# Kernel optimization log

Measured on AMD Instinct MI355X. Metric: run time of the kernel, lower is better.

The kernel has to match this reference:

```python
import jax, jax.numpy as jnp
import numpy as np

TEMPERATURE = 0.5  # set externally on the torch module; fixed here
EPS = 1e-10

B, NPTS, NDIM = 8, 1024, 64
K, S = 16, 512  # n_clusters, book_size


def setup_inputs() -> dict:
    key = jax.random.key(0)
    k1, k2, k3, k4 = jax.random.split(key, 4)
    ze = jax.random.normal(k1, (B, NPTS, NDIM), dtype=jnp.float32)
    # per-sample cluster probabilities (rows sum to 1)
    c_probs = jax.nn.softmax(jax.random.normal(k2, (B, K), dtype=jnp.float32), axis=-1)
    books = jax.random.normal(k3, (K, S, NDIM), dtype=jnp.float32)
    log_param_q = jnp.asarray(np.log(1.0), dtype=jnp.float32)  # param_q_init = 1.0
    gumbel_u = jax.random.uniform(k4, (B, K, NPTS, S), dtype=jnp.float32)
    return {"ze": ze, "c_probs": c_probs, "books": books,
            "log_param_q": log_param_q, "gumbel_u": gumbel_u}


def reference(ze, c_probs, books, log_param_q, gumbel_u):
    # precision of the Gaussian quantizer
    precision_q = 0.5 / jnp.clip(jnp.exp(log_param_q), 1e-10)
    # squared euclidean distances: [b, k, n, s]
    d = (jnp.sum(ze * ze, axis=-1)[:, None, :, None]
         + jnp.sum(books * books, axis=-1)[None, :, None, :]
         - 2.0 * jnp.einsum('bnd,ksd->bkns', ze, books))
    logits = -d * precision_q                                   # [b,k,n,s]
    # gumbel-softmax sample (training branch)
    g = -jnp.log(-jnp.log(gumbel_u + EPS) + EPS)
    encodings = jax.nn.softmax((logits + g) / TEMPERATURE, axis=-1)
    # soft codebook lookup, mixed over clusters by per-sample c_probs
    zq = jnp.einsum('bkns,ksd,bk->bnd', encodings, books, c_probs)
    prob = jax.nn.softmax(logits, axis=-1)
    log_prob = jax.nn.log_softmax(logits, axis=-1)
    return (zq, precision_q, prob, log_prob)
```

## Files before the change

### kernel.cpp

```cpp
#include <hip/hip_runtime.h>
#include <hip/hip_bf16.h>

typedef __attribute__((ext_vector_type(8))) short short8;
typedef __attribute__((ext_vector_type(4))) float f32x4;
typedef __attribute__((ext_vector_type(2))) float f32x2;

#define WS_ZE     0u
#define WS_B1H    (1u<<20)
#define WS_B2     (2u<<20)
#define WS_ZN2    (3u<<20)
#define WS_BS2    ((3u<<20)+32768u)
#define WS_ZQP    (4u<<20)

__device__ __forceinline__ unsigned short f2bf(float x) {
  __hip_bfloat16 h = __float2bfloat16(x);
  return __builtin_bit_cast(unsigned short, h);
}
__device__ __forceinline__ void lds_barrier() {
  asm volatile("s_waitcnt lgkmcnt(0)" ::: "memory");
  __builtin_amdgcn_s_barrier();
}

__global__ __launch_bounds__(256) void prep_all_k(const float* __restrict__ ze,
                                                  const float* __restrict__ books,
                                                  const float* __restrict__ lpq,
                                                  char* __restrict__ ws,
                                                  float* __restrict__ d_out) {
  const int bb = blockIdx.x;
  if (bb < 32) {
    int t = bb * 256 + threadIdx.x;
    const f32x4* row = (const f32x4*)(ze + t * 64);
    unsigned short* dh = (unsigned short*)(ws + WS_ZE) + t * 64;
    float s = 0.f;
#pragma unroll
    for (int c = 0; c < 8; ++c) {
      const f32x4 v0 = row[2 * c], v1 = row[2 * c + 1];
      union { unsigned short u[8]; short8 v; } H;
#pragma unroll
      for (int r = 0; r < 4; ++r) {
        float a = v0[r]; s += a * a; H.u[r] = f2bf(a);
        float b = v1[r]; s += b * b; H.u[4 + r] = f2bf(b);
      }
      *(short8*)(dh + c * 8) = H.v;
    }
    ((float*)(ws + WS_ZN2))[t] = s;
  } else if (bb < 64) {
    int t = (bb - 32) * 256 + threadIdx.x;
    if (t == 0) d_out[524288] = 0.5f / fmaxf(expf(lpq[0]), 1e-10f);
    const f32x4* row = (const f32x4*)(books + t * 64);
    float s = 0.f;
#pragma unroll
    for (int c = 0; c < 16; ++c) {
      const f32x4 v = row[c];
#pragma unroll
      for (int r = 0; r < 4; ++r) s += v[r] * v[r];
    }
    ((float*)(ws + WS_BS2))[t] = s;
  } else if (bb < 320) {
    int t = (bb - 64) * 256 + threadIdx.x;
    const int sl = t & 15, g = (t >> 4) & 3, f = (t >> 6) & 1, tt = (t >> 7) & 31, k = t >> 12;
    const float* src = books + ((k * 512 + tt * 16 + sl) * 64 + f * 32 + g * 8);
    const f32x4 v0 = *(const f32x4*)(src);
    const f32x4 v1 = *(const f32x4*)(src + 4);
    union { unsigned short u[8]; short8 v; } H;
#pragma unroll
    for (int r = 0; r < 4; ++r) { H.u[r] = f2bf(v0[r]); H.u[4 + r] = f2bf(v1[r]); }
    *(short8*)(ws + WS_B1H + (k * 32 + tt) * 2048 + f * 1024 + (sl + g * 16) * 16) = H.v;
  } else {
    int t = (bb - 320) * 256 + threadIdx.x;
    const int l15 = t & 15, sub = (t >> 4) & 3, m = (t >> 6) & 3, w = (t >> 8) & 7,
              hh = (t >> 11) & 1, k = t >> 12;
    const float* src = books + ((k * 512 + hh * 256 + w * 32 + sub * 8) * 64 + m * 16 + l15);
    union { unsigned short u[8]; short8 v; } H;
#pragma unroll
    for (int j = 0; j < 8; ++j) H.u[j] = f2bf(src[j * 64]);
    *(short8*)(ws + WS_B2 + k * 65536 + ((hh * 8 + w) * 4 + m) * 1024 + (l15 + sub * 16) * 16) = H.v;
  }
}

__global__ __launch_bounds__(256) void zq_red_k(const char* __restrict__ ws,
                                                float* __restrict__ d_out) {
  int t = blockIdx.x * 256 + threadIdx.x;
  const f32x4 a = *(const f32x4*)(ws + WS_ZQP + t * 16);
  const f32x4 b = *(const f32x4*)(ws + WS_ZQP + (2u << 20) + t * 16);
  const f32x4 c = *(const f32x4*)(ws + WS_ZQP + (4u << 20) + t * 16);
  const f32x4 d = *(const f32x4*)(ws + WS_ZQP + (6u << 20) + t * 16);
  *(f32x4*)(d_out + t * 4) = (a + b) + (c + d);
}

__global__ __launch_bounds__(512, 4)
void gvq_main(const float* __restrict__ gum, const float* __restrict__ cprobs,
              const float* __restrict__ lpq, char* __restrict__ ws,
              float* __restrict__ d_out) {
  __shared__ char lds[33088];
  char* lgb = lds;
  float* scr_esc = (float*)(lds + 33024);

  const int tid  = threadIdx.x;
  const int lane = tid & 63;
  const int wave = tid >> 6;
  const int l15  = lane & 15;
  const int g4   = lane >> 4;

  const int bid = blockIdx.x;
  const unsigned kg = ((unsigned)bid & 7u) >> 1;
  const int bt  = ((bid >> 3) << 1) | (bid & 1);
  const int b   = bt >> 6;
  const int n0  = (bt & 63) * 16;
  const int kbeg = (int)kg * 4;

  const float prec  = 0.5f / fmaxf(expf(lpq[0]), 1e-10f);
  const float prec2 = 2.0f * prec;
  const float C24   = 3.7751345442790977e-11f;

  const unsigned short* zh = (const unsigned short*)(ws + WS_ZE) + (b * 1024 + n0 + l15) * 64;
  const short8 zf0h = *(const short8*)(zh + g4 * 8);
  const short8 zf1h = *(const short8*)(zh + 32 + g4 * 8);
  const float zn2p = ((const float*)(ws + WS_ZN2))[b * 1024 + n0 + l15] * prec;

  f32x4 zacc[4] = {{0,0,0,0},{0,0,0,0},{0,0,0,0},{0,0,0,0}};

  const int nr0 = wave * 2, nr1 = wave * 2 + 1;

#pragma unroll 1
  for (int kk = 0; kk < 4; ++kk) {
    const int k = kbeg + kk;
    const float cp = cprobs[b * 16 + k];
    const char* b1h = ws + WS_B1H + k * 65536;
    const char* b2  = ws + WS_B2  + k * 65536;
    const float* bs2k = (const float*)(ws + WS_BS2) + k * 512;
    const long row0 = ((long)((b * 16 + k) * 1024) + n0 + nr0) * 512;
    const long row1 = ((long)((b * 16 + k) * 1024) + n0 + nr1) * 512;

#pragma unroll
    for (int i = 0; i < 4; ++i) {
      const int t = wave * 4 + i;
      const char* bh = b1h + t * 2048 + lane * 16;
      const short8 a0h = *(const short8*)(bh);
      const short8 a1h = *(const short8*)(bh + 1024);
      f32x4 c = {0.f, 0.f, 0.f, 0.f};
      c = __builtin_amdgcn_mfma_f32_16x16x32_bf16(a0h, zf0h, c, 0, 0, 0);
      c = __builtin_amdgcn_mfma_f32_16x16x32_bf16(a1h, zf1h, c, 0, 0, 0);
      const f32x4 bs2v = *(const f32x4*)(bs2k + t * 16 + g4 * 4);
      f32x4 lv;
#pragma unroll
      for (int r = 0; r < 4; ++r)
        lv[r] = fmaf(c[r], prec2, fmaf(bs2v[r], -prec, -zn2p));
      *(f32x4*)(lgb + l15 * 2064 + (t * 16 + g4 * 4) * 4) = lv;
    }
    lds_barrier();

#pragma unroll
    for (int r = 0; r < 2; ++r) {
      const int n = r ? nr1 : nr0;
      const long rowb = r ? row1 : row0;
      float uv[8];
#pragma unroll
      for (int j = 0; j < 8; ++j)
        uv[j] = __builtin_nontemporal_load(gum + rowb + j * 64 + lane);

      float Lv[8];
      const float* l32 = (const float*)(lgb + n * 2064);
#pragma unroll
      for (int j = 0; j < 8; ++j) Lv[j] = l32[j * 64 + lane];

      float m = Lv[0];
#pragma unroll
      for (int j = 1; j < 8; ++j) m = fmaxf(m, Lv[j]);
#pragma unroll
      for (int o = 1; o < 64; o <<= 1) m = fmaxf(m, __shfl_xor(m, o));

      unsigned short* er = (unsigned short*)(lgb + n * 2064);
      float z1 = 0.f, z2 = 0.f;
#pragma unroll
      for (int j = 0; j < 8; ++j) {
        const float e1 = __expf(Lv[j] - m); z1 += e1;
        const float L  = 1e-10f - __logf(uv[j] + 1e-10f);
        const float rl = __builtin_amdgcn_rcpf(L);
        const float e2 = (e1 * e1) * (rl * rl) * C24;
        z2 += e2;
        er[j * 64 + lane] = f2bf(e2);
      }
#pragma unroll
      for (int o = 1; o < 64; o <<= 1) {
        z1 += __shfl_xor(z1, o);
        z2 += __shfl_xor(z2, o);
      }
      const float c1 = m + __logf(z1);
      if (lane == 0) scr_esc[n] = cp / z2;

      float* pp = d_out + 524289 + rowb;
      float* pl = pp + 67108864;
#pragma unroll
      for (int j = 0; j < 8; ++j) {
        const float lpv = Lv[j] - c1;
        __builtin_nontemporal_store(__expf(lpv), pp + j * 64 + lane);
        __builtin_nontemporal_store(lpv, pl + j * 64 + lane);
      }
    }
    lds_barrier();

    {
      f32x4 cacc[4] = {{0,0,0,0},{0,0,0,0},{0,0,0,0},{0,0,0,0}};
#pragma unroll
      for (int h = 0; h < 2; ++h) {
        const short8 bf = *(const short8*)(lgb + l15 * 2064 +
                                           (h * 256 + wave * 32 + g4 * 8) * 2);
        const char* afb = b2 + ((h * 8 + wave) * 4) * 1024 + lane * 16;
#pragma unroll
        for (int m = 0; m < 4; ++m) {
          const short8 af = *(const short8*)(afb + m * 1024);
          cacc[m] = __builtin_amdgcn_mfma_f32_16x16x32_bf16(af, bf, cacc[m], 0, 0, 0);
        }
      }
      const float esc = scr_esc[l15];
#pragma unroll
      for (int m = 0; m < 4; ++m)
#pragma unroll
        for (int r = 0; r < 4; ++r) zacc[m][r] = fmaf(cacc[m][r], esc, zacc[m][r]);
    }
    lds_barrier();
  }

  __syncthreads();
#pragma unroll
  for (int m = 0; m < 4; ++m)
    *(f32x4*)(lds + wave * 4096 + l15 * 256 + m * 64 + g4 * 16) = zacc[m];
  __syncthreads();
  const int e = tid * 2;
  f32x2 acc = {0.f, 0.f};
#pragma unroll
  for (int w = 0; w < 8; ++w) acc += *(const f32x2*)(lds + w * 4096 + e * 4);
  *(f32x2*)(ws + WS_ZQP + kg * (2u << 20) +
            (((unsigned)(b * 1024 + n0)) * 64 + e) * 4) = acc;
}

extern "C" void kernel_launch(void* const* d_in, const int* in_sizes, int n_in,
                              void* d_out, int out_size, void* d_ws, size_t ws_size,
                              hipStream_t stream) {
  (void)in_sizes; (void)n_in; (void)out_size; (void)ws_size;
  const float* ze     = (const float*)d_in[0];
  const float* cprobs = (const float*)d_in[1];
  const float* books  = (const float*)d_in[2];
  const float* lpq    = (const float*)d_in[3];
  const float* gum    = (const float*)d_in[4];
  float* out = (float*)d_out;
  char* ws = (char*)d_ws;
  hipLaunchKernelGGL(prep_all_k, dim3(576),  dim3(256), 0, stream, ze, books, lpq, ws, out);
  hipLaunchKernelGGL(gvq_main,   dim3(2048), dim3(512), 0, stream, gum, cprobs, lpq, ws, out);
  hipLaunchKernelGGL(zq_red_k,   dim3(512),  dim3(256), 0, stream, ws, out);
}
```

Before: 230.5 us.

## Double row tile per block to 32 rows with 1024-thread blocks

Each main-kernel block now covers 32 points instead of 16, using 16 waves where two groups of 8 waves each handle 16 rows. The block count halves, so codebook fragments loaded per block are shared across twice as many rows, and LDS doubles to hold 32 logit rows. This cuts redundant codebook and bs2 global reads and the number of block launches. In exchange blocks get larger and barriers cover more waves, which may reduce scheduling flexibility and occupancy.

```diff
diff --git a/kernel.cpp b/kernel.cpp
--- a/kernel.cpp
+++ b/kernel.cpp
@@ -88,35 +88,38 @@
   *(f32x4*)(d_out + t * 4) = (a + b) + (c + d);
 }
 
-__global__ __launch_bounds__(512, 4)
+__global__ __launch_bounds__(1024, 2)
 void gvq_main(const float* __restrict__ gum, const float* __restrict__ cprobs,
               const float* __restrict__ lpq, char* __restrict__ ws,
               float* __restrict__ d_out) {
-  __shared__ char lds[33088];
+  __shared__ char lds[66176];
   char* lgb = lds;
-  float* scr_esc = (float*)(lds + 33024);
+  float* scr_esc = (float*)(lds + 66048);
 
   const int tid  = threadIdx.x;
   const int lane = tid & 63;
   const int wave = tid >> 6;
+  const int w8   = wave & 7;
+  const int nh   = wave >> 3;
   const int l15  = lane & 15;
   const int g4   = lane >> 4;
 
   const int bid = blockIdx.x;
-  const unsigned kg = ((unsigned)bid & 7u) >> 1;
-  const int bt  = ((bid >> 3) << 1) | (bid & 1);
-  const int b   = bt >> 6;
-  const int n0  = (bt & 63) * 16;
+  const unsigned kg = (unsigned)bid & 3u;
+  const int bt  = bid >> 2;
+  const int b   = bt >> 5;
+  const int nt0 = (bt & 31) * 32;
   const int kbeg = (int)kg * 4;
 
   const float prec  = 0.5f / fmaxf(expf(lpq[0]), 1e-10f);
   const float prec2 = 2.0f * prec;
   const float C24   = 3.7751345442790977e-11f;
 
-  const unsigned short* zh = (const unsigned short*)(ws + WS_ZE) + (b * 1024 + n0 + l15) * 64;
+  const unsigned short* zh = (const unsigned short*)(ws + WS_ZE)
+      + (b * 1024 + nt0 + nh * 16 + l15) * 64;
   const short8 zf0h = *(const short8*)(zh + g4 * 8);
   const short8 zf1h = *(const short8*)(zh + 32 + g4 * 8);
-  const float zn2p = ((const float*)(ws + WS_ZN2))[b * 1024 + n0 + l15] * prec;
+  const float zn2p = ((const float*)(ws + WS_ZN2))[b * 1024 + nt0 + nh * 16 + l15] * prec;
 
   f32x4 zacc[4] = {{0,0,0,0},{0,0,0,0},{0,0,0,0},{0,0,0,0}};
 
@@ -129,12 +132,12 @@
     const char* b1h = ws + WS_B1H + k * 65536;
     const char* b2  = ws + WS_B2  + k * 65536;
     const float* bs2k = (const float*)(ws + WS_BS2) + k * 512;
-    const long row0 = ((long)((b * 16 + k) * 1024) + n0 + nr0) * 512;
-    const long row1 = ((long)((b * 16 + k) * 1024) + n0 + nr1) * 512;
+    const long row0 = ((long)((b * 16 + k) * 1024) + nt0 + nr0) * 512;
+    const long row1 = ((long)((b * 16 + k) * 1024) + nt0 + nr1) * 512;
 
 #pragma unroll
     for (int i = 0; i < 4; ++i) {
-      const int t = wave * 4 + i;
+      const int t = w8 * 4 + i;
       const char* bh = b1h + t * 2048 + lane * 16;
       const short8 a0h = *(const short8*)(bh);
       const short8 a1h = *(const short8*)(bh + 1024);
@@ -146,7 +149,7 @@
 #pragma unroll
       for (int r = 0; r < 4; ++r)
         lv[r] = fmaf(c[r], prec2, fmaf(bs2v[r], -prec, -zn2p));
-      *(f32x4*)(lgb + l15 * 2064 + (t * 16 + g4 * 4) * 4) = lv;
+      *(f32x4*)(lgb + (nh * 16 + l15) * 2064 + (t * 16 + g4 * 4) * 4) = lv;
     }
     lds_barrier();
 
@@ -204,16 +207,16 @@
       f32x4 cacc[4] = {{0,0,0,0},{0,0,0,0},{0,0,0,0},{0,0,0,0}};
 #pragma unroll
       for (int h = 0; h < 2; ++h) {
-        const short8 bf = *(const short8*)(lgb + l15 * 2064 +
-                                           (h * 256 + wave * 32 + g4 * 8) * 2);
-        const char* afb = b2 + ((h * 8 + wave) * 4) * 1024 + lane * 16;
+        const short8 bf = *(const short8*)(lgb + (nh * 16 + l15) * 2064 +
+                                           (h * 256 + w8 * 32 + g4 * 8) * 2);
+        const char* afb = b2 + ((h * 8 + w8) * 4) * 1024 + lane * 16;
 #pragma unroll
         for (int m = 0; m < 4; ++m) {
           const short8 af = *(const short8*)(afb + m * 1024);
           cacc[m] = __builtin_amdgcn_mfma_f32_16x16x32_bf16(af, bf, cacc[m], 0, 0, 0);
         }
       }
-      const float esc = scr_esc[l15];
+      const float esc = scr_esc[nh * 16 + l15];
 #pragma unroll
       for (int m = 0; m < 4; ++m)
 #pragma unroll
@@ -228,11 +231,14 @@
     *(f32x4*)(lds + wave * 4096 + l15 * 256 + m * 64 + g4 * 16) = zacc[m];
   __syncthreads();
   const int e = tid * 2;
+  const int nn = e >> 6, d4 = (e & 63) * 4;
+  const int base = (nn >> 4) * 8;
   f32x2 acc = {0.f, 0.f};
 #pragma unroll
-  for (int w = 0; w < 8; ++w) acc += *(const f32x2*)(lds + w * 4096 + e * 4);
+  for (int w = 0; w < 8; ++w)
+    acc += *(const f32x2*)(lds + (base + w) * 4096 + (nn & 15) * 256 + d4);
   *(f32x2*)(ws + WS_ZQP + kg * (2u << 20) +
-            (((unsigned)(b * 1024 + n0)) * 64 + e) * 4) = acc;
+            (((unsigned)(b * 1024 + nt0)) * 64 + e) * 4) = acc;
 }
 
 extern "C" void kernel_launch(void* const* d_in, const int* in_sizes, int n_in,
@@ -246,7 +252,7 @@
   const float* gum    = (const float*)d_in[4];
   float* out = (float*)d_out;
   char* ws = (char*)d_ws;
-  hipLaunchKernelGGL(prep_all_k, dim3(576),  dim3(256), 0, stream, ze, books, lpq, ws, out);
-  hipLaunchKernelGGL(gvq_main,   dim3(2048), dim3(512), 0, stream, gum, cprobs, lpq, ws, out);
-  hipLaunchKernelGGL(zq_red_k,   dim3(512),  dim3(256), 0, stream, ws, out);
-}
+  hipLaunchKernelGGL(prep_all_k, dim3(576),  dim3(256),  0, stream, ze, books, lpq, ws, out);
+  hipLaunchKernelGGL(gvq_main,   dim3(1024), dim3(1024), 0, stream, gum, cprobs, lpq, ws, out);
+  hipLaunchKernelGGL(zq_red_k,   dim3(512),  dim3(256),  0, stream, ws, out);
+}
```

Result: slower. 239.4 us (+3.9%).

## Split clusters into three groups and prefetch next gumbel rows during MFMA

Applied to the files above, without the earlier changes.

The 16 clusters are now split across three block groups (6/5/5) instead of four groups of 4, so the grid shrinks to 1536 blocks and launch bounds drop to 3 blocks per CU. The zq partial reduction sums three partials instead of four. The gumbel loads for the next cluster are issued before the codebook-lookup MFMA phase so their latency overlaps compute. The cost is more registers held live for the prefetched rows and an uneven work split across groups.

```diff
diff --git a/kernel.cpp b/kernel.cpp
--- a/kernel.cpp
+++ b/kernel.cpp
@@ -84,11 +84,10 @@
   const f32x4 a = *(const f32x4*)(ws + WS_ZQP + t * 16);
   const f32x4 b = *(const f32x4*)(ws + WS_ZQP + (2u << 20) + t * 16);
   const f32x4 c = *(const f32x4*)(ws + WS_ZQP + (4u << 20) + t * 16);
-  const f32x4 d = *(const f32x4*)(ws + WS_ZQP + (6u << 20) + t * 16);
-  *(f32x4*)(d_out + t * 4) = (a + b) + (c + d);
-}
-
-__global__ __launch_bounds__(512, 4)
+  *(f32x4*)(d_out + t * 4) = a + b + c;
+}
+
+__global__ __launch_bounds__(512, 3)
 void gvq_main(const float* __restrict__ gum, const float* __restrict__ cprobs,
               const float* __restrict__ lpq, char* __restrict__ ws,
               float* __restrict__ d_out) {
@@ -103,11 +102,12 @@
   const int g4   = lane >> 4;
 
   const int bid = blockIdx.x;
-  const unsigned kg = ((unsigned)bid & 7u) >> 1;
-  const int bt  = ((bid >> 3) << 1) | (bid & 1);
+  const unsigned kg = (unsigned)bid % 3u;
+  const int bt  = (int)((unsigned)bid / 3u);
   const int b   = bt >> 6;
   const int n0  = (bt & 63) * 16;
-  const int kbeg = (int)kg * 4;
+  const int kbeg = (kg == 0) ? 0 : (kg == 1 ? 6 : 11);
+  const int kcnt = (kg == 0) ? 6 : 5;
 
   const float prec  = 0.5f / fmaxf(expf(lpq[0]), 1e-10f);
   const float prec2 = 2.0f * prec;
@@ -121,16 +121,30 @@
   f32x4 zacc[4] = {{0,0,0,0},{0,0,0,0},{0,0,0,0},{0,0,0,0}};
 
   const int nr0 = wave * 2, nr1 = wave * 2 + 1;
+  const long rowbase0 = ((long)(b * 16) * 1024 + n0 + nr0) * 512;
+  const long rowbase1 = ((long)(b * 16) * 1024 + n0 + nr1) * 512;
+
+  float uva[8], uvb[8];
+  {
+    const long r0 = rowbase0 + (long)kbeg * 524288;
+    const long r1 = rowbase1 + (long)kbeg * 524288;
+#pragma unroll
+    for (int j = 0; j < 8; ++j)
+      uva[j] = __builtin_nontemporal_load(gum + r0 + j * 64 + lane);
+#pragma unroll
+    for (int j = 0; j < 8; ++j)
+      uvb[j] = __builtin_nontemporal_load(gum + r1 + j * 64 + lane);
+  }
 
 #pragma unroll 1
-  for (int kk = 0; kk < 4; ++kk) {
+  for (int kk = 0; kk < kcnt; ++kk) {
     const int k = kbeg + kk;
     const float cp = cprobs[b * 16 + k];
     const char* b1h = ws + WS_B1H + k * 65536;
     const char* b2  = ws + WS_B2  + k * 65536;
     const float* bs2k = (const float*)(ws + WS_BS2) + k * 512;
-    const long row0 = ((long)((b * 16 + k) * 1024) + n0 + nr0) * 512;
-    const long row1 = ((long)((b * 16 + k) * 1024) + n0 + nr1) * 512;
+    const long row0 = rowbase0 + (long)k * 524288;
+    const long row1 = rowbase1 + (long)k * 524288;
 
 #pragma unroll
     for (int i = 0; i < 4; ++i) {
@@ -154,10 +168,6 @@
     for (int r = 0; r < 2; ++r) {
       const int n = r ? nr1 : nr0;
       const long rowb = r ? row1 : row0;
-      float uv[8];
-#pragma unroll
-      for (int j = 0; j < 8; ++j)
-        uv[j] = __builtin_nontemporal_load(gum + rowb + j * 64 + lane);
 
       float Lv[8];
       const float* l32 = (const float*)(lgb + n * 2064);
@@ -174,8 +184,9 @@
       float z1 = 0.f, z2 = 0.f;
 #pragma unroll
       for (int j = 0; j < 8; ++j) {
+        const float u = r ? uvb[j] : uva[j];
         const float e1 = __expf(Lv[j] - m); z1 += e1;
-        const float L  = 1e-10f - __logf(uv[j] + 1e-10f);
+        const float L  = 1e-10f - __logf(u + 1e-10f);
         const float rl = __builtin_amdgcn_rcpf(L);
         const float e2 = (e1 * e1) * (rl * rl) * C24;
         z2 += e2;
@@ -199,6 +210,17 @@
       }
     }
     lds_barrier();
+
+    if (kk + 1 < kcnt) {
+      const long rn0 = rowbase0 + (long)(k + 1) * 524288;
+      const long rn1 = rowbase1 + (long)(k + 1) * 524288;
+#pragma unroll
+      for (int j = 0; j < 8; ++j)
+        uva[j] = __builtin_nontemporal_load(gum + rn0 + j * 64 + lane);
+#pragma unroll
+      for (int j = 0; j < 8; ++j)
+        uvb[j] = __builtin_nontemporal_load(gum + rn1 + j * 64 + lane);
+    }
 
     {
       f32x4 cacc[4] = {{0,0,0,0},{0,0,0,0},{0,0,0,0},{0,0,0,0}};
@@ -247,6 +269,6 @@
   float* out = (float*)d_out;
   char* ws = (char*)d_ws;
   hipLaunchKernelGGL(prep_all_k, dim3(576),  dim3(256), 0, stream, ze, books, lpq, ws, out);
-  hipLaunchKernelGGL(gvq_main,   dim3(2048), dim3(512), 0, stream, gum, cprobs, lpq, ws, out);
+  hipLaunchKernelGGL(gvq_main,   dim3(1536), dim3(512), 0, stream, gum, cprobs, lpq, ws, out);
   hipLaunchKernelGGL(zq_red_k,   dim3(512),  dim3(256), 0, stream, ws, out);
 }
```

After: 237.9 us. 3.2% more time.
